# Kernel tuning notes

Hardware: AMD Instinct MI355X
Metric: run time of the kernel (lower is better)

The kernel has to match this reference:

```python
import jax, jax.numpy as jnp
import numpy as np

H = 128            # hardcoded image side in the torch module
TOL = 1e-3         # forward() default tol
MAX_DEPTH = 8      # init kwarg (reduced from 200 for bounded runtime)
LRELU = 0.1        # LeakyReLU negative slope


def _conv(x, w, b, pad):
    # x: [B,Cin,H,H], w: [Cout,Cin,kh,kw]
    y = jax.lax.conv_general_dilated(
        x, w, (1, 1), [(pad, pad), (pad, pad)],
        dimension_numbers=('NCHW', 'OIHW', 'NCHW'))
    if b is not None:
        y = y + b[None, :, None, None]
    return y


def _leaky(x):
    return jnp.where(x >= 0, x, LRELU * x)


def _build_apply_T(d, A, w1, b1, w2, b2, w3, b3, wK, delta, alpha, lambd, beta):
    B = d.shape[0]
    Kc = wK.shape[0]
    dcol = d.reshape(B, -1).T                      # [m, B]
    # ConvTranspose2d(K->1, k=3, pad=1) with weight := convK.weight is the
    # adjoint of convK: regular conv with spatially flipped, channel-swapped kernel.
    wKt = jnp.transpose(jnp.flip(wK, (2, 3)), (1, 0, 2, 3))  # [1,K,3,3]

    def K_op(xk):                                  # [N,B] -> [K*N,B]
        x4 = xk.T.reshape(B, 1, H, H)
        return _conv(x4, wK, None, 1).reshape(B, -1).T

    def Kt_op(pk):                                 # [K*N,B] -> [N,B]
        p4 = pk.T.reshape(B, Kc, H, H)
        return _conv(p4, wKt, None, 1).reshape(B, -1).T

    def R_op(pk):                                  # learned residual denoiser
        p = pk.T.reshape(B, Kc, H, H)
        p = p + _leaky(_conv(p, w1, b1, 2))
        p = p + _leaky(_conv(p, w2, b2, 2))
        p = p + _leaky(_conv(p, w3, b3, 2))
        return p.reshape(B, -1).T

    def ball_proj(w):                              # eval-mode projection
        de = jnp.exp(delta)                        # (1,) -> broadcasts over batch
        dist = jnp.maximum(jnp.linalg.norm(w - dcol, axis=0), 1e-10)
        dn = jnp.linalg.norm(dcol, axis=0)
        scale = jnp.minimum(jnp.ones_like(dist), de * dn / dist)
        return dcol + scale * (w - dcol)

    a = jnp.clip(alpha, 0.0, 2.0)
    bta = jnp.clip(beta, 0.0, 2.0)
    lam = jnp.clip(lambd, 0.0, 2.0)

    def apply_T(x):                                # x: [B,1,H,H]
        xk = x.reshape(B, -1).T                    # [N,B]
        Kxk = K_op(xk)
        # torch: pk = K(xk); pk += lambd*(nuk1 + alpha*(K(xk)-pk)) with nuk1=0
        # and pk==K(xk), so the update is identity -> pk = Kxk.
        pk = R_op(Kxk)
        Axk = A @ xk                               # [m,B]
        # torch: wk = A@xk; temp = wk + lambd*(nuk2 + alpha*(Axk-wk)) = Axk.
        wk = ball_proj(Axk)
        nuk1p = a * (Kxk - pk)
        nuk2p = a * (Axk - wk)
        # nuk1 = nuk2 = 0, so 2*nuk_plus - nuk = 2*nuk_plus
        rk = Kt_op(2.0 * nuk1p) + A.T @ (2.0 * nuk2p)
        xk_new = jnp.clip(xk - bta * rk, 0.0, 1.0)
        return xk_new.T.reshape(B, 1, H, H)

    return apply_T


def setup_inputs() -> dict:
    key = jax.random.key(0)
    ks = jax.random.split(key, 10)
    B, M, N_side, Kc = 8, 4096, 128, 2
    d = jax.random.normal(ks[0], (B, M), jnp.float32)
    A = jax.random.normal(ks[1], (M, N_side * N_side), jnp.float32) / 128.0
    w1 = jax.random.normal(ks[2], (Kc, Kc, 5, 5), jnp.float32) * 0.05
    w2 = jax.random.normal(ks[3], (Kc, Kc, 5, 5), jnp.float32) * 0.05
    w3 = jax.random.normal(ks[4], (Kc, Kc, 5, 5), jnp.float32) * 0.05
    b1 = jnp.zeros((Kc,), jnp.float32)
    b2 = jnp.zeros((Kc,), jnp.float32)
    b3 = jnp.zeros((Kc,), jnp.float32)
    wK = jax.random.normal(ks[5], (Kc, 1, 3, 3), jnp.float32) * 0.1
    return {
        'd': d, 'A': A,
        'w1': w1, 'b1': b1, 'w2': w2, 'b2': b2, 'w3': w3, 'b3': b3,
        'wK': wK,
        'delta': jnp.full((1,), -5.0, jnp.float32),
        'alpha': jnp.full((1,), 0.1, jnp.float32),
        'lambd': jnp.full((1,), 0.1, jnp.float32),
        'beta': jnp.full((1,), 0.1, jnp.float32),
    }


def reference(d, A, w1, b1, w2, b2, w3, b3, wK, delta, alpha, lambd, beta):
    B = d.shape[0]
    apply_T = _build_apply_T(d, A, w1, b1, w2, b2, w3, b3, wK,
                             delta, alpha, lambd, beta)
    x0 = jnp.zeros((B, 1, H, H), d.dtype)
    xp0 = jnp.full((B, 1, H, H), jnp.inf, d.dtype)

    def cond(state):
        x, xp, k = state
        res = jnp.max(jnp.linalg.norm((x - xp).reshape(B, -1), axis=1))
        return (res > TOL) & (k < MAX_DEPTH)

    def body(state):
        x, xp, k = state
        return (apply_T(x), x, k + 1)

    x_star, _, _ = jax.lax.while_loop(cond, body, (x0, xp0, jnp.int32(0)))
    # final differentiable application T(x*)
    return apply_T(x_star)
```

## Files before the change

### kernel.cpp

```cpp
#include <hip/hip_runtime.h>
#include <math.h>

#define HH 128
#define NPIX 16384
#define BB 8
#define MM 4096
#define NN 16384
#define LRELU_S 0.1f

typedef __attribute__((ext_vector_type(8))) short bf16x8;
typedef __attribute__((ext_vector_type(4))) float f32x4;

__device__ __forceinline__ float leaky_(float v){ return v >= 0.f ? v : LRELU_S*v; }
__device__ __forceinline__ float clamp01(float v){ return fminf(fmaxf(v, 0.f), 1.f); }
__device__ __forceinline__ float clamp02(float v){ return fminf(fmaxf(v, 0.f), 2.f); }
__device__ __forceinline__ unsigned short f2bf(float f){
  unsigned u = __float_as_uint(f);
  u = (u + 0x7FFFu + ((u >> 16) & 1u)) >> 16;
  return (unsigned short)u;
}
__device__ __forceinline__ float bf2f(unsigned short s){
  return __uint_as_float(((unsigned)s) << 16);
}

__global__ __launch_bounds__(256) void k_prep(const float* __restrict__ A_,
                                              unsigned short* __restrict__ Abf){
  size_t i = ((size_t)blockIdx.x*256 + threadIdx.x)*8;
  float4 v0 = *(const float4*)&A_[i];
  float4 v1 = *(const float4*)&A_[i+4];
  unsigned short o[8] = { f2bf(v0.x), f2bf(v0.y), f2bf(v0.z), f2bf(v0.w),
                          f2bf(v1.x), f2bf(v1.y), f2bf(v1.z), f2bf(v1.w) };
  *(uint4*)&Abf[i] = *(uint4*)o;
}

__global__ __launch_bounds__(256) void k_dn(const float* __restrict__ d, float* __restrict__ dn){
  int b = blockIdx.x, t = threadIdx.x;
  float ss = 0.f;
  for (int m=t; m<MM; m+=256){ float v = d[b*MM + m]; ss += v*v; }
  #pragma unroll
  for (int off=32; off; off>>=1) ss += __shfl_down(ss, off);
  __shared__ float red[4];
  if ((t & 63) == 0) red[t>>6] = ss;
  __syncthreads();
  if (t == 0) dn[b] = sqrtf(red[0]+red[1]+red[2]+red[3]);
}

__global__ __launch_bounds__(256) void k_conv_chain(const float* __restrict__ x,
    const float* __restrict__ wK, const float* __restrict__ w1, const float* __restrict__ b1,
    const float* __restrict__ w2, const float* __restrict__ b2,
    const float* __restrict__ w3, const float* __restrict__ b3,
    const float* __restrict__ alpha, float* __restrict__ rk){
  __shared__ float xs[24][128];
  __shared__ float bufA[2][22][128];
  __shared__ float bufB[2][18][128];
  __shared__ float wKs[18], w1s[100], w2s[100], w3s[100], bs[3][2];
  __shared__ float twoa;
  int blk = blockIdx.x;
  int b = blk >> 4, slab = blk & 15, r0 = slab*8;
  int t = threadIdx.x;
  for (int i=t;i<18;i+=256) wKs[i]=wK[i];
  for (int i=t;i<100;i+=256){ w1s[i]=w1[i]; w2s[i]=w2[i]; w3s[i]=w3[i]; }
  if (t<2){ bs[0][t]=b1[t]; bs[1][t]=b2[t]; bs[2][t]=b3[t]; }
  if (t==0) twoa = 2.f*clamp02(alpha[0]);
  for (int idx=t; idx<24*128; idx+=256){
    int i = idx>>7, j = idx&127, ir = r0-8+i;
    xs[i][j] = ((unsigned)ir < 128u) ? x[b*NPIX + ir*HH + j] : 0.f;
  }
  __syncthreads();
  for (int c=0;c<2;++c)
    for (int idx=t; idx<22*128; idx+=256){
      int i = idx>>7, j = idx&127, ir = r0-7+i;
      float s = 0.f;
      if ((unsigned)ir < 128u){
        #pragma unroll
        for (int di=0;di<3;++di)
          #pragma unroll
          for (int dj=0;dj<3;++dj){
            int jj = j+dj-1;
            if ((unsigned)jj < 128u) s += xs[i+di][jj]*wKs[(c*3+di)*3+dj];
          }
      }
      bufA[c][i][j] = s;
    }
  __syncthreads();
  for (int o=0;o<2;++o)
    for (int idx=t; idx<18*128; idx+=256){
      int i = idx>>7, j = idx&127, ir = r0-5+i;
      float v = 0.f;
      if ((unsigned)ir < 128u){
        float s = bs[0][o];
        #pragma unroll
        for (int c=0;c<2;++c)
          #pragma unroll
          for (int di=0;di<5;++di)
            #pragma unroll
            for (int dj=0;dj<5;++dj){
              int jj = j+dj-2;
              if ((unsigned)jj < 128u) s += bufA[c][i+di][jj]*w1s[(o*2+c)*25+di*5+dj];
            }
        v = bufA[o][i+2][j] + leaky_(s);
      }
      bufB[o][i][j] = v;
    }
  __syncthreads();
  for (int o=0;o<2;++o)
    for (int idx=t; idx<14*128; idx+=256){
      int i = idx>>7, j = idx&127, ir = r0-3+i;
      float v = 0.f;
      if ((unsigned)ir < 128u){
        float s = bs[1][o];
        #pragma unroll
        for (int c=0;c<2;++c)
          #pragma unroll
          for (int di=0;di<5;++di)
            #pragma unroll
            for (int dj=0;dj<5;++dj){
              int jj = j+dj-2;
              if ((unsigned)jj < 128u) s += bufB[c][i+di][jj]*w2s[(o*2+c)*25+di*5+dj];
            }
        v = bufB[o][i+2][j] + leaky_(s);
      }
      bufA[o][i][j] = v;
    }
  __syncthreads();
  for (int o=0;o<2;++o)
    for (int idx=t; idx<10*128; idx+=256){
      int i = idx>>7, j = idx&127, ir = r0-1+i;
      float v = 0.f;
      if ((unsigned)ir < 128u){
        float s = bs[2][o];
        #pragma unroll
        for (int c=0;c<2;++c)
          #pragma unroll
          for (int di=0;di<5;++di)
            #pragma unroll
            for (int dj=0;dj<5;++dj){
              int jj = j+dj-2;
              if ((unsigned)jj < 128u) s += bufA[c][i+di][jj]*w3s[(o*2+c)*25+di*5+dj];
            }
        v = bufA[o][i+2][j] + leaky_(s);
      }
      bufB[o][i][j] = v;
    }
  __syncthreads();
  for (int c=0;c<2;++c)
    for (int idx=t; idx<10*128; idx+=256){
      int i = idx>>7, j = idx&127, ir = r0-1+i;
      float v = 0.f;
      if ((unsigned)ir < 128u){
        float kx = 0.f;
        #pragma unroll
        for (int di=0;di<3;++di)
          #pragma unroll
          for (int dj=0;dj<3;++dj){
            int jj = j+dj-1;
            if ((unsigned)jj < 128u) kx += xs[i+6+di][jj]*wKs[(c*3+di)*3+dj];
          }
        v = twoa*(kx - bufB[c][i][j]);
      }
      bufA[c][i][j] = v;
    }
  __syncthreads();
  for (int idx=t; idx<8*128; idx+=256){
    int i = idx>>7, j = idx&127, ir = r0+i;
    float s = 0.f;
    #pragma unroll
    for (int c=0;c<2;++c)
      #pragma unroll
      for (int di=0;di<3;++di)
        #pragma unroll
        for (int dj=0;dj<3;++dj){
          int jj = j+dj-1;
          if ((unsigned)jj < 128u) s += bufA[c][i+di][jj]*wKs[(c*3+(2-di))*3+(2-dj)];
        }
    rk[b*NPIX + ir*HH + j] = s;
  }
}

__global__ __launch_bounds__(512) void k_gemm1mf(const unsigned short* __restrict__ Abf,
    const unsigned short* __restrict__ xtt, const float* __restrict__ d_,
    float* __restrict__ e_, float* __restrict__ d2p){
  int mt = blockIdx.x;
  int w = threadIdx.x >> 6;
  int lane = threadIdx.x & 63;
  int kg = lane >> 4, col = lane & 15;
  const unsigned short* Ap = Abf + (size_t)(mt*16 + col)*NN + w*2048 + kg*8;
  const unsigned short* Bp = xtt + ((size_t)(w*256 + kg)*16 + col)*8;
  f32x4 acc = {0.f,0.f,0.f,0.f};
  #pragma unroll 8
  for (int s=0; s<64; ++s){
    bf16x8 a = *(const bf16x8*)(Ap + s*32);
    bf16x8 b = *(const bf16x8*)(Bp + s*512);
    acc = __builtin_amdgcn_mfma_f32_16x16x32_bf16(a, b, acc, 0, 0, 0);
  }
  __shared__ float part[8][16][16];
  __shared__ float p2[16][16];
  #pragma unroll
  for (int j=0;j<4;++j) part[w][kg*4+j][col] = acc[j];
  __syncthreads();
  int t = threadIdx.x;
  if (t < 256){
    int r = t >> 4, b = t & 15;
    float s = 0.f;
    #pragma unroll
    for (int w2=0; w2<8; ++w2) s += part[w2][r][b];
    int m = mt*16 + r;
    float ee = s - ((b < 8) ? d_[b*MM + m] : 0.f);
    e_[m*16 + b] = ee;
    p2[r][b] = (b < 8) ? ee*ee : 0.f;
  }
  __syncthreads();
  if (t < 8){
    float s2 = 0.f;
    #pragma unroll
    for (int r2=0;r2<16;++r2) s2 += p2[r2][t];
    d2p[mt*8 + t] = s2;
  }
}

#define G2_MS 32
#define G2_MC 128
#define G2_NB 16
#define G2_NC 1024
__global__ __launch_bounds__(256) void k_gemm2v(const unsigned short* __restrict__ Abf,
    const float* __restrict__ e_, const float* __restrict__ d2p,
    const float* __restrict__ dn, const float* __restrict__ delta,
    const float* __restrict__ alpha, float* __restrict__ up){
  __shared__ float zs[BB][G2_MC];
  __shared__ float red[8][8];
  __shared__ float cf[8];
  int blk = blockIdx.x;
  int ms = blk >> 4, nb = blk & 15;
  int m0 = ms*G2_MC, n0 = nb*G2_NC;
  int t = threadIdx.x;
  if (t < 64){
    int b = t & 7, part = t >> 3;
    float s = 0.f;
    for (int i=0;i<32;++i) s += d2p[(part*32+i)*8 + b];
    red[part][b] = s;
  }
  __syncthreads();
  if (t < 8){
    float s2 = 0.f;
    #pragma unroll
    for (int p=0;p<8;++p) s2 += red[p][t];
    float dist = fmaxf(sqrtf(s2), 1e-10f);
    float de = expf(delta[0]);
    float a = clamp02(alpha[0]);
    cf[t] = 2.f*a*(1.f - fminf(1.f, de*dn[t]/dist));
  }
  __syncthreads();
  for (int i=t; i<BB*G2_MC; i+=256){
    int ml = i >> 3, b = i & 7;
    zs[b][ml] = cf[b]*e_[(m0+ml)*16 + b];
  }
  __syncthreads();
  float4 acc[BB];
  #pragma unroll
  for (int b=0;b<BB;++b){ acc[b].x=0.f; acc[b].y=0.f; acc[b].z=0.f; acc[b].w=0.f; }
  const unsigned short* Ap = Abf + (size_t)m0*NN + n0 + t*4;
  #pragma unroll 4
  for (int ml=0; ml<G2_MC; ++ml){
    uint2 araw = *(const uint2*)(Ap + (size_t)ml*NN);
    float a0 = bf2f((unsigned short)(araw.x & 0xffff));
    float a1 = bf2f((unsigned short)(araw.x >> 16));
    float a2 = bf2f((unsigned short)(araw.y & 0xffff));
    float a3 = bf2f((unsigned short)(araw.y >> 16));
    #pragma unroll
    for (int b=0;b<BB;++b){
      float s = zs[b][ml];
      acc[b].x += a0*s; acc[b].y += a1*s; acc[b].z += a2*s; acc[b].w += a3*s;
    }
  }
  #pragma unroll
  for (int b=0;b<BB;++b)
    *(float4*)&up[((size_t)ms*BB + b)*NN + n0 + t*4] = acc[b];
}

__global__ __launch_bounds__(256) void k_combine2(const float* __restrict__ up,
    const float* __restrict__ rk, const float* __restrict__ beta,
    float* __restrict__ x, unsigned short* __restrict__ xtt){
  int gid = blockIdx.x*256 + threadIdx.x;
  int b = gid >> 11, nb = gid & 2047, n0 = nb*8;
  if (b >= 8){
    uint4 z = {0,0,0,0};
    *(uint4*)&xtt[(size_t)(nb*16 + b)*8] = z;
    return;
  }
  float bta = clamp02(beta[0]);
  float acc[8];
  {
    float4 r0 = *(const float4*)&rk[b*NPIX + n0];
    float4 r1 = *(const float4*)&rk[b*NPIX + n0 + 4];
    acc[0]=r0.x; acc[1]=r0.y; acc[2]=r0.z; acc[3]=r0.w;
    acc[4]=r1.x; acc[5]=r1.y; acc[6]=r1.z; acc[7]=r1.w;
  }
  #pragma unroll 8
  for (int ms=0; ms<G2_MS; ++ms){
    const float* u = &up[((size_t)ms*BB + b)*NN + n0];
    float4 u0 = *(const float4*)u;
    float4 u1 = *(const float4*)(u+4);
    acc[0]+=u0.x; acc[1]+=u0.y; acc[2]+=u0.z; acc[3]+=u0.w;
    acc[4]+=u1.x; acc[5]+=u1.y; acc[6]+=u1.z; acc[7]+=u1.w;
  }
  float xv[8]; unsigned short o[8];
  #pragma unroll
  for (int j=0;j<8;++j){
    xv[j] = clamp01(x[b*NPIX + n0 + j] - bta*acc[j]);
    o[j] = f2bf(xv[j]);
  }
  #pragma unroll
  for (int j=0;j<8;++j) x[b*NPIX + n0 + j] = xv[j];
  *(uint4*)&xtt[(size_t)(nb*16 + b)*8] = *(uint4*)o;
}

extern "C" void kernel_launch(void* const* d_in, const int* in_sizes, int n_in,
                              void* d_out, int out_size, void* d_ws, size_t ws_size,
                              hipStream_t stream) {
  const float* d_d   = (const float*)d_in[0];
  const float* d_A   = (const float*)d_in[1];
  const float* w1    = (const float*)d_in[2];
  const float* b1    = (const float*)d_in[3];
  const float* w2    = (const float*)d_in[4];
  const float* b2    = (const float*)d_in[5];
  const float* w3    = (const float*)d_in[6];
  const float* b3    = (const float*)d_in[7];
  const float* wK    = (const float*)d_in[8];
  const float* delta = (const float*)d_in[9];
  const float* alpha = (const float*)d_in[10];
  const float* beta  = (const float*)d_in[12];

  char* p = (char*)d_ws;
  unsigned short* Abf = (unsigned short*)p; p += (size_t)MM*NN*2;
  unsigned short* xtt = (unsigned short*)p; p += (size_t)2048*16*8*2;
  float* x   = (float*)p; p += (size_t)BB*NPIX*4;
  float* rk1 = (float*)p; p += (size_t)BB*NPIX*4;
  float* e_  = (float*)p; p += (size_t)MM*16*4;
  float* up  = (float*)p; p += (size_t)G2_MS*BB*NN*4;
  float* d2p = (float*)p; p += (size_t)256*8*4;
  float* dnb = (float*)p; p += 64;

  k_prep<<<MM*NN/(256*8), 256, 0, stream>>>(d_A, Abf);
  k_dn<<<BB, 256, 0, stream>>>(d_d, dnb);
  hipMemsetAsync(x, 0, (size_t)BB*NPIX*4, stream);
  hipMemsetAsync(xtt, 0, (size_t)2048*16*8*2, stream);

  for (int it=0; it<9; ++it){
    k_conv_chain<<<128, 256, 0, stream>>>(x, wK, w1, b1, w2, b2, w3, b3, alpha, rk1);
    k_gemm1mf<<<256, 512, 0, stream>>>(Abf, xtt, d_d, e_, d2p);
    k_gemm2v<<<G2_MS*G2_NB, 256, 0, stream>>>(Abf, e_, d2p, dnb, delta, alpha, up);
    k_combine2<<<128, 256, 0, stream>>>(up, rk1, beta, x, xtt);
  }

  hipMemcpyAsync(d_out, x, (size_t)BB*NPIX*4, hipMemcpyDeviceToDevice, stream);
}
```

Before: 1.498 ms.

## Fuse A^T GEMM with combine step and stage gemm1 A tiles through LDS

Gemm1 now loads A rows into swizzled shared memory with direct global-to-LDS loads, using 4 waves per block instead of 8 waves reading global memory directly. Gemm2 is restructured so each block owns 64 columns and loops over all of M, reducing in-block and applying the clamp/x update directly. This removes the split-M partial buffer and the separate combine kernel along with its traffic. The cost is far fewer independent blocks for gemm2 (256 blocks, each streaming all of M with a sync per chunk) and narrow 4-byte A loads, so bandwidth utilisation may drop.

```diff
diff --git a/kernel.cpp b/kernel.cpp
--- a/kernel.cpp
+++ b/kernel.cpp
@@ -10,6 +10,8 @@
 
 typedef __attribute__((ext_vector_type(8))) short bf16x8;
 typedef __attribute__((ext_vector_type(4))) float f32x4;
+typedef __attribute__((address_space(3))) unsigned int as3_u32;
+typedef __attribute__((address_space(1))) const unsigned int as1_u32;
 
 __device__ __forceinline__ float leaky_(float v){ return v >= 0.f ? v : LRELU_S*v; }
 __device__ __forceinline__ float clamp01(float v){ return fminf(fmaxf(v, 0.f), 1.f); }
@@ -177,34 +179,48 @@
   }
 }
 
-__global__ __launch_bounds__(512) void k_gemm1mf(const unsigned short* __restrict__ Abf,
+__global__ __launch_bounds__(256) void k_gemm1s(const unsigned short* __restrict__ Abf,
     const unsigned short* __restrict__ xtt, const float* __restrict__ d_,
     float* __restrict__ e_, float* __restrict__ d2p){
+  __shared__ char tileb[32768];
+  __shared__ float part[4][16][16];
+  __shared__ float p2[16][16];
   int mt = blockIdx.x;
-  int w = threadIdx.x >> 6;
-  int lane = threadIdx.x & 63;
+  int m0 = mt*16;
+  int t = threadIdx.x;
+  int w = t >> 6, lane = t & 63;
   int kg = lane >> 4, col = lane & 15;
-  const unsigned short* Ap = Abf + (size_t)(mt*16 + col)*NN + w*2048 + kg*8;
-  const unsigned short* Bp = xtt + ((size_t)(w*256 + kg)*16 + col)*8;
   f32x4 acc = {0.f,0.f,0.f,0.f};
-  #pragma unroll 8
-  for (int s=0; s<64; ++s){
-    bf16x8 a = *(const bf16x8*)(Ap + s*32);
-    bf16x8 b = *(const bf16x8*)(Bp + s*512);
-    acc = __builtin_amdgcn_mfma_f32_16x16x32_bf16(a, b, acc, 0, 0, 0);
-  }
-  __shared__ float part[8][16][16];
-  __shared__ float p2[16][16];
+
+  for (int c=0; c<16; ++c){
+    if (c) __syncthreads();
+    #pragma unroll
+    for (int q=0; q<8; ++q){
+      int kk = w*8 + q;
+      int row = kk >> 1;
+      int kb = (kk & 1)*1024 + lane*16;
+      int cb = kb ^ ((row & 7) << 4);
+      const unsigned short* gp = Abf + (size_t)(m0+row)*NN + c*1024 + (cb>>1);
+      __builtin_amdgcn_global_load_lds((as1_u32*)gp,
+          (as3_u32*)&tileb[kk*1024], 16, 0, 0);
+    }
+    __syncthreads();
+    #pragma unroll
+    for (int j=0; j<8; ++j){
+      int cbyte = w*512 + j*64 + kg*16;
+      bf16x8 a = *(const bf16x8*)&tileb[col*2048 + (cbyte ^ ((col & 7) << 4))];
+      int nbase = c*1024 + w*256 + j*32;
+      bf16x8 b = *(const bf16x8*)(xtt + ((size_t)(nbase>>3) + kg)*128 + col*8);
+      acc = __builtin_amdgcn_mfma_f32_16x16x32_bf16(a, b, acc, 0, 0, 0);
+    }
+  }
   #pragma unroll
   for (int j=0;j<4;++j) part[w][kg*4+j][col] = acc[j];
   __syncthreads();
-  int t = threadIdx.x;
-  if (t < 256){
+  {
     int r = t >> 4, b = t & 15;
-    float s = 0.f;
-    #pragma unroll
-    for (int w2=0; w2<8; ++w2) s += part[w2][r][b];
-    int m = mt*16 + r;
+    float s = part[0][r][b] + part[1][r][b] + part[2][r][b] + part[3][r][b];
+    int m = m0 + r;
     float ee = s - ((b < 8) ? d_[b*MM + m] : 0.f);
     e_[m*16 + b] = ee;
     p2[r][b] = (b < 8) ? ee*ee : 0.f;
@@ -218,100 +234,86 @@
   }
 }
 
-#define G2_MS 32
-#define G2_MC 128
-#define G2_NB 16
-#define G2_NC 1024
-__global__ __launch_bounds__(256) void k_gemm2v(const unsigned short* __restrict__ Abf,
+__global__ __launch_bounds__(256) void k_gemm2c(const unsigned short* __restrict__ Abf,
     const float* __restrict__ e_, const float* __restrict__ d2p,
     const float* __restrict__ dn, const float* __restrict__ delta,
-    const float* __restrict__ alpha, float* __restrict__ up){
-  __shared__ float zs[BB][G2_MC];
-  __shared__ float red[8][8];
+    const float* __restrict__ alpha, const float* __restrict__ beta,
+    const float* __restrict__ rk, float* __restrict__ x,
+    unsigned short* __restrict__ xtt){
+  __shared__ float zs[8][64];
+  __shared__ float red8[8][8];
   __shared__ float cf[8];
+  __shared__ float redbuf[8][32][16];
   int blk = blockIdx.x;
-  int ms = blk >> 4, nb = blk & 15;
-  int m0 = ms*G2_MC, n0 = nb*G2_NC;
+  int n0 = blk*64;
   int t = threadIdx.x;
   if (t < 64){
-    int b = t & 7, part = t >> 3;
+    int b = t & 7, prt = t >> 3;
     float s = 0.f;
-    for (int i=0;i<32;++i) s += d2p[(part*32+i)*8 + b];
-    red[part][b] = s;
+    for (int i=0;i<32;++i) s += d2p[(prt*32+i)*8 + b];
+    red8[prt][b] = s;
   }
   __syncthreads();
   if (t < 8){
     float s2 = 0.f;
     #pragma unroll
-    for (int p=0;p<8;++p) s2 += red[p][t];
+    for (int p=0;p<8;++p) s2 += red8[p][t];
     float dist = fmaxf(sqrtf(s2), 1e-10f);
     float de = expf(delta[0]);
     float a = clamp02(alpha[0]);
     cf[t] = 2.f*a*(1.f - fminf(1.f, de*dn[t]/dist));
   }
   __syncthreads();
-  for (int i=t; i<BB*G2_MC; i+=256){
-    int ml = i >> 3, b = i & 7;
-    zs[b][ml] = cf[b]*e_[(m0+ml)*16 + b];
-  }
-  __syncthreads();
-  float4 acc[BB];
-  #pragma unroll
-  for (int b=0;b<BB;++b){ acc[b].x=0.f; acc[b].y=0.f; acc[b].z=0.f; acc[b].w=0.f; }
-  const unsigned short* Ap = Abf + (size_t)m0*NN + n0 + t*4;
-  #pragma unroll 4
-  for (int ml=0; ml<G2_MC; ++ml){
-    uint2 araw = *(const uint2*)(Ap + (size_t)ml*NN);
-    float a0 = bf2f((unsigned short)(araw.x & 0xffff));
-    float a1 = bf2f((unsigned short)(araw.x >> 16));
-    float a2 = bf2f((unsigned short)(araw.y & 0xffff));
-    float a3 = bf2f((unsigned short)(araw.y >> 16));
-    #pragma unroll
-    for (int b=0;b<BB;++b){
-      float s = zs[b][ml];
-      acc[b].x += a0*s; acc[b].y += a1*s; acc[b].z += a2*s; acc[b].w += a3*s;
-    }
-  }
-  #pragma unroll
-  for (int b=0;b<BB;++b)
-    *(float4*)&up[((size_t)ms*BB + b)*NN + n0 + t*4] = acc[b];
-}
-
-__global__ __launch_bounds__(256) void k_combine2(const float* __restrict__ up,
-    const float* __restrict__ rk, const float* __restrict__ beta,
-    float* __restrict__ x, unsigned short* __restrict__ xtt){
-  int gid = blockIdx.x*256 + threadIdx.x;
-  int b = gid >> 11, nb = gid & 2047, n0 = nb*8;
-  if (b >= 8){
-    uint4 z = {0,0,0,0};
-    *(uint4*)&xtt[(size_t)(nb*16 + b)*8] = z;
-    return;
-  }
+  int c2 = t & 31, r = t >> 5;
+  float acc[8][2];
+  #pragma unroll
+  for (int b=0;b<8;++b){ acc[b][0]=0.f; acc[b][1]=0.f; }
+  for (int mc=0; mc<64; ++mc){
+    __syncthreads();
+    {
+      int i0 = t*2;
+      int b0 = i0>>6, rl0 = i0&63;
+      zs[b0][rl0] = cf[b0]*e_[(size_t)(mc*64+rl0)*16 + b0];
+      int i1 = i0+1;
+      int b1 = i1>>6, rl1 = i1&63;
+      zs[b1][rl1] = cf[b1]*e_[(size_t)(mc*64+rl1)*16 + b1];
+    }
+    __syncthreads();
+    #pragma unroll
+    for (int rr=0; rr<8; ++rr){
+      int rowl = rr*8 + r;
+      unsigned a2 = *(const unsigned*)&Abf[(size_t)(mc*64+rowl)*NN + n0 + c2*2];
+      float a0 = bf2f((unsigned short)(a2 & 0xffff));
+      float a1 = bf2f((unsigned short)(a2 >> 16));
+      #pragma unroll
+      for (int b=0;b<8;++b){
+        float zv = zs[b][rowl];
+        acc[b][0] += a0*zv;
+        acc[b][1] += a1*zv;
+      }
+    }
+  }
+  __syncthreads();
+  #pragma unroll
+  for (int b=0;b<8;++b){
+    redbuf[r][c2][b*2]   = acc[b][0];
+    redbuf[r][c2][b*2+1] = acc[b][1];
+  }
+  __syncthreads();
   float bta = clamp02(beta[0]);
-  float acc[8];
-  {
-    float4 r0 = *(const float4*)&rk[b*NPIX + n0];
-    float4 r1 = *(const float4*)&rk[b*NPIX + n0 + 4];
-    acc[0]=r0.x; acc[1]=r0.y; acc[2]=r0.z; acc[3]=r0.w;
-    acc[4]=r1.x; acc[5]=r1.y; acc[6]=r1.z; acc[7]=r1.w;
-  }
-  #pragma unroll 8
-  for (int ms=0; ms<G2_MS; ++ms){
-    const float* u = &up[((size_t)ms*BB + b)*NN + n0];
-    float4 u0 = *(const float4*)u;
-    float4 u1 = *(const float4*)(u+4);
-    acc[0]+=u0.x; acc[1]+=u0.y; acc[2]+=u0.z; acc[3]+=u0.w;
-    acc[4]+=u1.x; acc[5]+=u1.y; acc[6]+=u1.z; acc[7]+=u1.w;
-  }
-  float xv[8]; unsigned short o[8];
-  #pragma unroll
-  for (int j=0;j<8;++j){
-    xv[j] = clamp01(x[b*NPIX + n0 + j] - bta*acc[j]);
-    o[j] = f2bf(xv[j]);
-  }
-  #pragma unroll
-  for (int j=0;j<8;++j) x[b*NPIX + n0 + j] = xv[j];
-  *(uint4*)&xtt[(size_t)(nb*16 + b)*8] = *(uint4*)o;
+  #pragma unroll
+  for (int vv=0; vv<2; ++vv){
+    int v = t*2 + vv;
+    int colv = v >> 3, b = v & 7;
+    int c2v = colv >> 1, sub = colv & 1;
+    float s = 0.f;
+    #pragma unroll
+    for (int rr=0;rr<8;++rr) s += redbuf[rr][c2v][b*2+sub];
+    int pix = n0 + colv;
+    float xn = clamp01(x[b*NPIX + pix] - bta*(rk[b*NPIX + pix] + s));
+    x[b*NPIX + pix] = xn;
+    xtt[((size_t)(pix>>3)*16 + b)*8 + (pix&7)] = f2bf(xn);
+  }
 }
 
 extern "C" void kernel_launch(void* const* d_in, const int* in_sizes, int n_in,
@@ -336,7 +338,6 @@
   float* x   = (float*)p; p += (size_t)BB*NPIX*4;
   float* rk1 = (float*)p; p += (size_t)BB*NPIX*4;
   float* e_  = (float*)p; p += (size_t)MM*16*4;
-  float* up  = (float*)p; p += (size_t)G2_MS*BB*NN*4;
   float* d2p = (float*)p; p += (size_t)256*8*4;
   float* dnb = (float*)p; p += 64;
 
@@ -347,9 +348,8 @@
 
   for (int it=0; it<9; ++it){
     k_conv_chain<<<128, 256, 0, stream>>>(x, wK, w1, b1, w2, b2, w3, b3, alpha, rk1);
-    k_gemm1mf<<<256, 512, 0, stream>>>(Abf, xtt, d_d, e_, d2p);
-    k_gemm2v<<<G2_MS*G2_NB, 256, 0, stream>>>(Abf, e_, d2p, dnb, delta, alpha, up);
-    k_combine2<<<128, 256, 0, stream>>>(up, rk1, beta, x, xtt);
+    k_gemm1s<<<256, 256, 0, stream>>>(Abf, xtt, d_d, e_, d2p);
+    k_gemm2c<<<256, 256, 0, stream>>>(Abf, e_, d2p, dnb, delta, alpha, beta, rk1, x, xtt);
   }
 
   hipMemcpyAsync(d_out, x, (size_t)BB*NPIX*4, hipMemcpyDeviceToDevice, stream);
```

Result: slower. 2.124 ms (+41.7%).

## Fuse iteration kernels into a persistent megakernel with grid barriers

Applied to the files above, without the earlier changes.

Replaces the four kernels launched per iteration (conv chain, first GEMM, second GEMM, combine) with one persistent 256-block kernel. The stages are separated by atomic grid-wide barriers, which removes 36 kernel launches and their gaps. Work is also repartitioned to fit 256 blocks: conv slabs of 4 rows, GEMM1 with 4 waves each covering a longer K range, and GEMM2 with 256-row M chunks so there are 16 partial sums instead of 32. The cost is larger conv halo overhead, fewer waves per block for GEMM1, and a dependence on all 256 blocks being co-resident, otherwise the barrier deadlocks.

```diff
diff --git a/kernel.cpp b/kernel.cpp
--- a/kernel.cpp
+++ b/kernel.cpp
@@ -7,6 +7,7 @@
 #define MM 4096
 #define NN 16384
 #define LRELU_S 0.1f
+#define NBLK 256
 
 typedef __attribute__((ext_vector_type(8))) short bf16x8;
 typedef __attribute__((ext_vector_type(4))) float f32x4;
@@ -45,273 +46,266 @@
   if (t == 0) dn[b] = sqrtf(red[0]+red[1]+red[2]+red[3]);
 }
 
-__global__ __launch_bounds__(256) void k_conv_chain(const float* __restrict__ x,
+__device__ __forceinline__ void gbar(int* cnt, unsigned* gen){
+  __syncthreads();
+  if (threadIdx.x == 0){
+    __threadfence();
+    unsigned g = __hip_atomic_load(gen, __ATOMIC_RELAXED, __HIP_MEMORY_SCOPE_AGENT);
+    int a = __hip_atomic_fetch_add(cnt, 1, __ATOMIC_ACQ_REL, __HIP_MEMORY_SCOPE_AGENT);
+    if (a == NBLK-1){
+      __hip_atomic_store(cnt, 0, __ATOMIC_RELAXED, __HIP_MEMORY_SCOPE_AGENT);
+      __hip_atomic_store(gen, g+1u, __ATOMIC_RELEASE, __HIP_MEMORY_SCOPE_AGENT);
+    } else {
+      while (__hip_atomic_load(gen, __ATOMIC_ACQUIRE, __HIP_MEMORY_SCOPE_AGENT) == g)
+        __builtin_amdgcn_s_sleep(4);
+    }
+    __threadfence();
+  }
+  __syncthreads();
+}
+
+__global__ __launch_bounds__(256) void k_mega(
+    const unsigned short* __restrict__ Abf, const float* __restrict__ d_,
     const float* __restrict__ wK, const float* __restrict__ w1, const float* __restrict__ b1,
     const float* __restrict__ w2, const float* __restrict__ b2,
     const float* __restrict__ w3, const float* __restrict__ b3,
-    const float* __restrict__ alpha, float* __restrict__ rk){
-  __shared__ float xs[24][128];
-  __shared__ float bufA[2][22][128];
-  __shared__ float bufB[2][18][128];
-  __shared__ float wKs[18], w1s[100], w2s[100], w3s[100], bs[3][2];
-  __shared__ float twoa;
-  int blk = blockIdx.x;
-  int b = blk >> 4, slab = blk & 15, r0 = slab*8;
-  int t = threadIdx.x;
+    const float* __restrict__ delta, const float* __restrict__ alpha,
+    const float* __restrict__ beta, const float* __restrict__ dn,
+    float* __restrict__ x, unsigned short* __restrict__ xtt,
+    float* __restrict__ rk1, float* __restrict__ e_, float* __restrict__ d2p,
+    float* __restrict__ up, int* bar_cnt, unsigned* bar_gen){
+  __shared__ float smem[10752];
+  __shared__ float wKs[18], w1s[100], w2s[100], w3s[100], bs[6], cf_s[8], red8s[64];
+  __shared__ float scal[2];
+  int blk = blockIdx.x, t = threadIdx.x;
+  float (*xs)[128]   = (float(*)[128])&smem[0];
+  float (*bufA)[18][128] = (float(*)[18][128])&smem[2560];
+  float (*bufB)[14][128] = (float(*)[14][128])&smem[7168];
+  float (*part)[16][16] = (float(*)[16][16])&smem[0];
+  float (*p2)[16] = (float(*)[16])&smem[1024];
+  float (*zs)[256] = (float(*)[256])&smem[0];
+
   for (int i=t;i<18;i+=256) wKs[i]=wK[i];
   for (int i=t;i<100;i+=256){ w1s[i]=w1[i]; w2s[i]=w2[i]; w3s[i]=w3[i]; }
-  if (t<2){ bs[0][t]=b1[t]; bs[1][t]=b2[t]; bs[2][t]=b3[t]; }
-  if (t==0) twoa = 2.f*clamp02(alpha[0]);
-  for (int idx=t; idx<24*128; idx+=256){
-    int i = idx>>7, j = idx&127, ir = r0-8+i;
-    xs[i][j] = ((unsigned)ir < 128u) ? x[b*NPIX + ir*HH + j] : 0.f;
-  }
+  if (t<2){ bs[t]=b1[t]; bs[2+t]=b2[t]; bs[4+t]=b3[t]; }
+  if (t==0){ scal[0] = 2.f*clamp02(alpha[0]); scal[1] = clamp02(beta[0]); }
   __syncthreads();
-  for (int c=0;c<2;++c)
-    for (int idx=t; idx<22*128; idx+=256){
-      int i = idx>>7, j = idx&127, ir = r0-7+i;
-      float s = 0.f;
-      if ((unsigned)ir < 128u){
-        #pragma unroll
-        for (int di=0;di<3;++di)
-          #pragma unroll
-          for (int dj=0;dj<3;++dj){
-            int jj = j+dj-1;
-            if ((unsigned)jj < 128u) s += xs[i+di][jj]*wKs[(c*3+di)*3+dj];
-          }
-      }
-      bufA[c][i][j] = s;
-    }
-  __syncthreads();
-  for (int o=0;o<2;++o)
-    for (int idx=t; idx<18*128; idx+=256){
-      int i = idx>>7, j = idx&127, ir = r0-5+i;
-      float v = 0.f;
-      if ((unsigned)ir < 128u){
-        float s = bs[0][o];
+
+  for (int it=0; it<9; ++it){
+    {
+      int b = blk >> 5, slab = blk & 31, r0 = slab*4;
+      for (int idx=t; idx<20*128; idx+=256){
+        int i = idx>>7, j = idx&127, ir = r0-8+i;
+        xs[i][j] = ((unsigned)ir < 128u) ? x[b*NPIX + ir*HH + j] : 0.f;
+      }
+      __syncthreads();
+      for (int c=0;c<2;++c)
+        for (int idx=t; idx<18*128; idx+=256){
+          int i = idx>>7, j = idx&127, ir = r0-7+i;
+          float s = 0.f;
+          if ((unsigned)ir < 128u){
+            #pragma unroll
+            for (int di=0;di<3;++di)
+              #pragma unroll
+              for (int dj=0;dj<3;++dj){
+                int jj = j+dj-1;
+                if ((unsigned)jj < 128u) s += xs[i+di][jj]*wKs[(c*3+di)*3+dj];
+              }
+          }
+          bufA[c][i][j] = s;
+        }
+      __syncthreads();
+      for (int o=0;o<2;++o)
+        for (int idx=t; idx<14*128; idx+=256){
+          int i = idx>>7, j = idx&127, ir = r0-5+i;
+          float v = 0.f;
+          if ((unsigned)ir < 128u){
+            float s = bs[o];
+            #pragma unroll
+            for (int c=0;c<2;++c)
+              #pragma unroll
+              for (int di=0;di<5;++di)
+                #pragma unroll
+                for (int dj=0;dj<5;++dj){
+                  int jj = j+dj-2;
+                  if ((unsigned)jj < 128u) s += bufA[c][i+di][jj]*w1s[(o*2+c)*25+di*5+dj];
+                }
+            v = bufA[o][i+2][j] + leaky_(s);
+          }
+          bufB[o][i][j] = v;
+        }
+      __syncthreads();
+      for (int o=0;o<2;++o)
+        for (int idx=t; idx<10*128; idx+=256){
+          int i = idx>>7, j = idx&127, ir = r0-3+i;
+          float v = 0.f;
+          if ((unsigned)ir < 128u){
+            float s = bs[2+o];
+            #pragma unroll
+            for (int c=0;c<2;++c)
+              #pragma unroll
+              for (int di=0;di<5;++di)
+                #pragma unroll
+                for (int dj=0;dj<5;++dj){
+                  int jj = j+dj-2;
+                  if ((unsigned)jj < 128u) s += bufB[c][i+di][jj]*w2s[(o*2+c)*25+di*5+dj];
+                }
+            v = bufB[o][i+2][j] + leaky_(s);
+          }
+          bufA[o][i][j] = v;
+        }
+      __syncthreads();
+      for (int o=0;o<2;++o)
+        for (int idx=t; idx<6*128; idx+=256){
+          int i = idx>>7, j = idx&127, ir = r0-1+i;
+          float v = 0.f;
+          if ((unsigned)ir < 128u){
+            float s = bs[4+o];
+            #pragma unroll
+            for (int c=0;c<2;++c)
+              #pragma unroll
+              for (int di=0;di<5;++di)
+                #pragma unroll
+                for (int dj=0;dj<5;++dj){
+                  int jj = j+dj-2;
+                  if ((unsigned)jj < 128u) s += bufA[c][i+di][jj]*w3s[(o*2+c)*25+di*5+dj];
+                }
+            v = bufA[o][i+2][j] + leaky_(s);
+          }
+          bufB[o][i][j] = v;
+        }
+      __syncthreads();
+      for (int c=0;c<2;++c)
+        for (int idx=t; idx<6*128; idx+=256){
+          int i = idx>>7, j = idx&127, ir = r0-1+i;
+          float v = 0.f;
+          if ((unsigned)ir < 128u){
+            float kx = 0.f;
+            #pragma unroll
+            for (int di=0;di<3;++di)
+              #pragma unroll
+              for (int dj=0;dj<3;++dj){
+                int jj = j+dj-1;
+                if ((unsigned)jj < 128u) kx += xs[i+6+di][jj]*wKs[(c*3+di)*3+dj];
+              }
+            v = scal[0]*(kx - bufB[c][i][j]);
+          }
+          bufA[c][i][j] = v;
+        }
+      __syncthreads();
+      for (int idx=t; idx<4*128; idx+=256){
+        int i = idx>>7, j = idx&127, ir = r0+i;
+        float s = 0.f;
         #pragma unroll
         for (int c=0;c<2;++c)
           #pragma unroll
-          for (int di=0;di<5;++di)
-            #pragma unroll
-            for (int dj=0;dj<5;++dj){
-              int jj = j+dj-2;
-              if ((unsigned)jj < 128u) s += bufA[c][i+di][jj]*w1s[(o*2+c)*25+di*5+dj];
+          for (int di=0;di<3;++di)
+            #pragma unroll
+            for (int dj=0;dj<3;++dj){
+              int jj = j+dj-1;
+              if ((unsigned)jj < 128u) s += bufA[c][i+di][jj]*wKs[(c*3+(2-di))*3+(2-dj)];
             }
-        v = bufA[o][i+2][j] + leaky_(s);
-      }
-      bufB[o][i][j] = v;
-    }
-  __syncthreads();
-  for (int o=0;o<2;++o)
-    for (int idx=t; idx<14*128; idx+=256){
-      int i = idx>>7, j = idx&127, ir = r0-3+i;
-      float v = 0.f;
-      if ((unsigned)ir < 128u){
-        float s = bs[1][o];
-        #pragma unroll
-        for (int c=0;c<2;++c)
-          #pragma unroll
-          for (int di=0;di<5;++di)
-            #pragma unroll
-            for (int dj=0;dj<5;++dj){
-              int jj = j+dj-2;
-              if ((unsigned)jj < 128u) s += bufB[c][i+di][jj]*w2s[(o*2+c)*25+di*5+dj];
-            }
-        v = bufB[o][i+2][j] + leaky_(s);
-      }
-      bufA[o][i][j] = v;
-    }
-  __syncthreads();
-  for (int o=0;o<2;++o)
-    for (int idx=t; idx<10*128; idx+=256){
-      int i = idx>>7, j = idx&127, ir = r0-1+i;
-      float v = 0.f;
-      if ((unsigned)ir < 128u){
-        float s = bs[2][o];
-        #pragma unroll
-        for (int c=0;c<2;++c)
-          #pragma unroll
-          for (int di=0;di<5;++di)
-            #pragma unroll
-            for (int dj=0;dj<5;++dj){
-              int jj = j+dj-2;
-              if ((unsigned)jj < 128u) s += bufA[c][i+di][jj]*w3s[(o*2+c)*25+di*5+dj];
-            }
-        v = bufA[o][i+2][j] + leaky_(s);
-      }
-      bufB[o][i][j] = v;
-    }
-  __syncthreads();
-  for (int c=0;c<2;++c)
-    for (int idx=t; idx<10*128; idx+=256){
-      int i = idx>>7, j = idx&127, ir = r0-1+i;
-      float v = 0.f;
-      if ((unsigned)ir < 128u){
-        float kx = 0.f;
-        #pragma unroll
-        for (int di=0;di<3;++di)
-          #pragma unroll
-          for (int dj=0;dj<3;++dj){
-            int jj = j+dj-1;
-            if ((unsigned)jj < 128u) kx += xs[i+6+di][jj]*wKs[(c*3+di)*3+dj];
-          }
-        v = twoa*(kx - bufB[c][i][j]);
-      }
-      bufA[c][i][j] = v;
-    }
-  __syncthreads();
-  for (int idx=t; idx<8*128; idx+=256){
-    int i = idx>>7, j = idx&127, ir = r0+i;
-    float s = 0.f;
-    #pragma unroll
-    for (int c=0;c<2;++c)
+        rk1[b*NPIX + ir*HH + j] = s;
+      }
+      __syncthreads();
+    }
+    {
+      int mt = blk;
+      int w = t >> 6, lane = t & 63;
+      int kg = lane >> 4, col = lane & 15;
+      const unsigned short* Ap = Abf + (size_t)(mt*16 + col)*NN + w*4096 + kg*8;
+      const unsigned short* Bp = xtt + ((size_t)(w*512 + kg)*16 + col)*8;
+      f32x4 acc = {0.f,0.f,0.f,0.f};
+      #pragma unroll 8
+      for (int s=0; s<128; ++s){
+        bf16x8 a = *(const bf16x8*)(Ap + s*32);
+        bf16x8 b = *(const bf16x8*)(Bp + s*512);
+        acc = __builtin_amdgcn_mfma_f32_16x16x32_bf16(a, b, acc, 0, 0, 0);
+      }
       #pragma unroll
-      for (int di=0;di<3;++di)
-        #pragma unroll
-        for (int dj=0;dj<3;++dj){
-          int jj = j+dj-1;
-          if ((unsigned)jj < 128u) s += bufA[c][i+di][jj]*wKs[(c*3+(2-di))*3+(2-dj)];
-        }
-    rk[b*NPIX + ir*HH + j] = s;
+      for (int j=0;j<4;++j) part[w][kg*4+j][col] = acc[j];
+      __syncthreads();
+      {
+        int r = t >> 4, b = t & 15;
+        float s = part[0][r][b] + part[1][r][b] + part[2][r][b] + part[3][r][b];
+        int m = mt*16 + r;
+        float ee = s - ((b < 8) ? d_[b*MM + m] : 0.f);
+        e_[m*16 + b] = ee;
+        p2[r][b] = (b < 8) ? ee*ee : 0.f;
+      }
+      __syncthreads();
+      if (t < 8){
+        float s2 = 0.f;
+        #pragma unroll
+        for (int r2=0;r2<16;++r2) s2 += p2[r2][t];
+        d2p[mt*8 + t] = s2;
+      }
+    }
+    gbar(bar_cnt, bar_gen);
+    {
+      if (t < 64){
+        int b = t & 7, prt = t >> 3;
+        float s = 0.f;
+        for (int i=0;i<32;++i) s += d2p[(prt*32+i)*8 + b];
+        red8s[prt*8 + b] = s;
+      }
+      __syncthreads();
+      if (t < 8){
+        float s2 = 0.f;
+        #pragma unroll
+        for (int p=0;p<8;++p) s2 += red8s[p*8 + t];
+        float dist = fmaxf(sqrtf(s2), 1e-10f);
+        float de = expf(delta[0]);
+        cf_s[t] = scal[0]*(1.f - fminf(1.f, de*dn[t]/dist));
+      }
+      __syncthreads();
+      int ms = blk >> 4, nb = blk & 15;
+      int m0 = ms*256, n0 = nb*1024;
+      for (int i=t; i<8*256; i+=256){
+        int ml = i >> 3, b = i & 7;
+        zs[b][ml] = cf_s[b]*e_[(size_t)(m0+ml)*16 + b];
+      }
+      __syncthreads();
+      float4 acc[BB];
+      #pragma unroll
+      for (int b=0;b<BB;++b){ acc[b].x=0.f; acc[b].y=0.f; acc[b].z=0.f; acc[b].w=0.f; }
+      const unsigned short* Ap = Abf + (size_t)m0*NN + n0 + t*4;
+      #pragma unroll 4
+      for (int ml=0; ml<256; ++ml){
+        uint2 araw = *(const uint2*)(Ap + (size_t)ml*NN);
+        float a0 = bf2f((unsigned short)(araw.x & 0xffff));
+        float a1 = bf2f((unsigned short)(araw.x >> 16));
+        float a2 = bf2f((unsigned short)(araw.y & 0xffff));
+        float a3 = bf2f((unsigned short)(araw.y >> 16));
+        #pragma unroll
+        for (int b=0;b<BB;++b){
+          float s = zs[b][ml];
+          acc[b].x += a0*s; acc[b].y += a1*s; acc[b].z += a2*s; acc[b].w += a3*s;
+        }
+      }
+      #pragma unroll
+      for (int b=0;b<BB;++b)
+        *(float4*)&up[((size_t)ms*BB + b)*NN + n0 + t*4] = acc[b];
+      __syncthreads();
+    }
+    gbar(bar_cnt, bar_gen);
+    {
+      float bta = scal[1];
+      #pragma unroll
+      for (int h=0; h<2; ++h){
+        int o = h*65536 + blk*256 + t;
+        int b = o >> 14, pix = o & 16383;
+        float s = rk1[b*NPIX + pix];
+        #pragma unroll
+        for (int ms=0; ms<16; ++ms)
+          s += up[((size_t)ms*BB + b)*NN + pix];
+        float xn = clamp01(x[b*NPIX + pix] - bta*s);
+        x[b*NPIX + pix] = xn;
+        xtt[((size_t)(pix>>3)*16 + b)*8 + (pix&7)] = f2bf(xn);
+      }
+    }
+    if (it < 8) gbar(bar_cnt, bar_gen);
   }
-}
-
-__global__ __launch_bounds__(512) void k_gemm1mf(const unsigned short* __restrict__ Abf,
-    const unsigned short* __restrict__ xtt, const float* __restrict__ d_,
-    float* __restrict__ e_, float* __restrict__ d2p){
-  int mt = blockIdx.x;
-  int w = threadIdx.x >> 6;
-  int lane = threadIdx.x & 63;
-  int kg = lane >> 4, col = lane & 15;
-  const unsigned short* Ap = Abf + (size_t)(mt*16 + col)*NN + w*2048 + kg*8;
-  const unsigned short* Bp = xtt + ((size_t)(w*256 + kg)*16 + col)*8;
-  f32x4 acc = {0.f,0.f,0.f,0.f};
-  #pragma unroll 8
-  for (int s=0; s<64; ++s){
-    bf16x8 a = *(const bf16x8*)(Ap + s*32);
-    bf16x8 b = *(const bf16x8*)(Bp + s*512);
-    acc = __builtin_amdgcn_mfma_f32_16x16x32_bf16(a, b, acc, 0, 0, 0);
-  }
-  __shared__ float part[8][16][16];
-  __shared__ float p2[16][16];
-  #pragma unroll
-  for (int j=0;j<4;++j) part[w][kg*4+j][col] = acc[j];
-  __syncthreads();
-  int t = threadIdx.x;
-  if (t < 256){
-    int r = t >> 4, b = t & 15;
-    float s = 0.f;
-    #pragma unroll
-    for (int w2=0; w2<8; ++w2) s += part[w2][r][b];
-    int m = mt*16 + r;
-    float ee = s - ((b < 8) ? d_[b*MM + m] : 0.f);
-    e_[m*16 + b] = ee;
-    p2[r][b] = (b < 8) ? ee*ee : 0.f;
-  }
-  __syncthreads();
-  if (t < 8){
-    float s2 = 0.f;
-    #pragma unroll
-    for (int r2=0;r2<16;++r2) s2 += p2[r2][t];
-    d2p[mt*8 + t] = s2;
-  }
-}
-
-#define G2_MS 32
-#define G2_MC 128
-#define G2_NB 16
-#define G2_NC 1024
-__global__ __launch_bounds__(256) void k_gemm2v(const unsigned short* __restrict__ Abf,
-    const float* __restrict__ e_, const float* __restrict__ d2p,
-    const float* __restrict__ dn, const float* __restrict__ delta,
-    const float* __restrict__ alpha, float* __restrict__ up){
-  __shared__ float zs[BB][G2_MC];
-  __shared__ float red[8][8];
-  __shared__ float cf[8];
-  int blk = blockIdx.x;
-  int ms = blk >> 4, nb = blk & 15;
-  int m0 = ms*G2_MC, n0 = nb*G2_NC;
-  int t = threadIdx.x;
-  if (t < 64){
-    int b = t & 7, part = t >> 3;
-    float s = 0.f;
-    for (int i=0;i<32;++i) s += d2p[(part*32+i)*8 + b];
-    red[part][b] = s;
-  }
-  __syncthreads();
-  if (t < 8){
-    float s2 = 0.f;
-    #pragma unroll
-    for (int p=0;p<8;++p) s2 += red[p][t];
-    float dist = fmaxf(sqrtf(s2), 1e-10f);
-    float de = expf(delta[0]);
-    float a = clamp02(alpha[0]);
-    cf[t] = 2.f*a*(1.f - fminf(1.f, de*dn[t]/dist));
-  }
-  __syncthreads();
-  for (int i=t; i<BB*G2_MC; i+=256){
-    int ml = i >> 3, b = i & 7;
-    zs[b][ml] = cf[b]*e_[(m0+ml)*16 + b];
-  }
-  __syncthreads();
-  float4 acc[BB];
-  #pragma unroll
-  for (int b=0;b<BB;++b){ acc[b].x=0.f; acc[b].y=0.f; acc[b].z=0.f; acc[b].w=0.f; }
-  const unsigned short* Ap = Abf + (size_t)m0*NN + n0 + t*4;
-  #pragma unroll 4
-  for (int ml=0; ml<G2_MC; ++ml){
-    uint2 araw = *(const uint2*)(Ap + (size_t)ml*NN);
-    float a0 = bf2f((unsigned short)(araw.x & 0xffff));
-    float a1 = bf2f((unsigned short)(araw.x >> 16));
-    float a2 = bf2f((unsigned short)(araw.y & 0xffff));
-    float a3 = bf2f((unsigned short)(araw.y >> 16));
-    #pragma unroll
-    for (int b=0;b<BB;++b){
-      float s = zs[b][ml];
-      acc[b].x += a0*s; acc[b].y += a1*s; acc[b].z += a2*s; acc[b].w += a3*s;
-    }
-  }
-  #pragma unroll
-  for (int b=0;b<BB;++b)
-    *(float4*)&up[((size_t)ms*BB + b)*NN + n0 + t*4] = acc[b];
-}
-
-__global__ __launch_bounds__(256) void k_combine2(const float* __restrict__ up,
-    const float* __restrict__ rk, const float* __restrict__ beta,
-    float* __restrict__ x, unsigned short* __restrict__ xtt){
-  int gid = blockIdx.x*256 + threadIdx.x;
-  int b = gid >> 11, nb = gid & 2047, n0 = nb*8;
-  if (b >= 8){
-    uint4 z = {0,0,0,0};
-    *(uint4*)&xtt[(size_t)(nb*16 + b)*8] = z;
-    return;
-  }
-  float bta = clamp02(beta[0]);
-  float acc[8];
-  {
-    float4 r0 = *(const float4*)&rk[b*NPIX + n0];
-    float4 r1 = *(const float4*)&rk[b*NPIX + n0 + 4];
-    acc[0]=r0.x; acc[1]=r0.y; acc[2]=r0.z; acc[3]=r0.w;
-    acc[4]=r1.x; acc[5]=r1.y; acc[6]=r1.z; acc[7]=r1.w;
-  }
-  #pragma unroll 8
-  for (int ms=0; ms<G2_MS; ++ms){
-    const float* u = &up[((size_t)ms*BB + b)*NN + n0];
-    float4 u0 = *(const float4*)u;
-    float4 u1 = *(const float4*)(u+4);
-    acc[0]+=u0.x; acc[1]+=u0.y; acc[2]+=u0.z; acc[3]+=u0.w;
-    acc[4]+=u1.x; acc[5]+=u1.y; acc[6]+=u1.z; acc[7]+=u1.w;
-  }
-  float xv[8]; unsigned short o[8];
-  #pragma unroll
-  for (int j=0;j<8;++j){
-    xv[j] = clamp01(x[b*NPIX + n0 + j] - bta*acc[j]);
-    o[j] = f2bf(xv[j]);
-  }
-  #pragma unroll
-  for (int j=0;j<8;++j) x[b*NPIX + n0 + j] = xv[j];
-  *(uint4*)&xtt[(size_t)(nb*16 + b)*8] = *(uint4*)o;
 }
 
 extern "C" void kernel_launch(void* const* d_in, const int* in_sizes, int n_in,
@@ -336,21 +330,21 @@
   float* x   = (float*)p; p += (size_t)BB*NPIX*4;
   float* rk1 = (float*)p; p += (size_t)BB*NPIX*4;
   float* e_  = (float*)p; p += (size_t)MM*16*4;
-  float* up  = (float*)p; p += (size_t)G2_MS*BB*NN*4;
+  float* up  = (float*)p; p += (size_t)16*BB*NN*4;
   float* d2p = (float*)p; p += (size_t)256*8*4;
   float* dnb = (float*)p; p += 64;
+  int* bar   = (int*)p;  p += 64;
 
   k_prep<<<MM*NN/(256*8), 256, 0, stream>>>(d_A, Abf);
   k_dn<<<BB, 256, 0, stream>>>(d_d, dnb);
   hipMemsetAsync(x, 0, (size_t)BB*NPIX*4, stream);
   hipMemsetAsync(xtt, 0, (size_t)2048*16*8*2, stream);
-
-  for (int it=0; it<9; ++it){
-    k_conv_chain<<<128, 256, 0, stream>>>(x, wK, w1, b1, w2, b2, w3, b3, alpha, rk1);
-    k_gemm1mf<<<256, 512, 0, stream>>>(Abf, xtt, d_d, e_, d2p);
-    k_gemm2v<<<G2_MS*G2_NB, 256, 0, stream>>>(Abf, e_, d2p, dnb, delta, alpha, up);
-    k_combine2<<<128, 256, 0, stream>>>(up, rk1, beta, x, xtt);
-  }
+  hipMemsetAsync(bar, 0, 8, stream);
+
+  k_mega<<<NBLK, 256, 0, stream>>>(Abf, d_d, wK, w1, b1, w2, b2, w3, b3,
+                                   delta, alpha, beta, dnb,
+                                   x, xtt, rk1, e_, d2p, up,
+                                   bar, (unsigned*)(bar+1));
 
   hipMemcpyAsync(d_out, x, (size_t)BB*NPIX*4, hipMemcpyDeviceToDevice, stream);
 }
```

Result: slower. 2.757 ms (+84.0%).
